# Kernel tuning notes

Hardware: AMD Instinct MI355X
Metric: run time of the kernel (lower is better)

The kernel has to match this reference:

```python
import jax, jax.numpy as jnp
import numpy as np
from jax import lax

K = 8  # number of KNN neighbors (excluding self)


def setup_inputs() -> dict:
    key = jax.random.key(0)
    k1, k2, k3 = jax.random.split(key, 3)
    B, H, W, C = 32, 14, 14, 2048
    OUT = 512
    x = jax.random.normal(k1, (B, H, W, C), dtype=jnp.float32)
    W1 = jax.random.normal(k2, (C, OUT), dtype=jnp.float32) * (1.0 / np.sqrt(C))
    b1 = jnp.zeros((OUT,), dtype=jnp.float32)
    W2 = jax.random.normal(k3, (OUT, OUT), dtype=jnp.float32) * (1.0 / np.sqrt(OUT))
    b2 = jnp.zeros((OUT,), dtype=jnp.float32)
    return {"x": x, "W1": W1, "b1": b1, "W2": W2, "b2": b2}


def _knn_edges(xf, k):
    # full pairwise squared-euclidean distance (monotone in cdist p=2)
    sq = jnp.sum(xf * xf, axis=-1)                      # [N]
    d2 = sq[:, None] + sq[None, :] - 2.0 * (xf @ xf.T)  # [N, N]
    _, idx = lax.top_k(-d2, k + 1)                      # smallest k+1
    knn = idx[:, 1:]                                    # drop self
    N = xf.shape[0]
    src = jnp.repeat(jnp.arange(N), k)
    dst = knn.reshape(-1)
    # GCNConv adds self-loops
    loops = jnp.arange(N)
    src = jnp.concatenate([src, loops])
    dst = jnp.concatenate([dst, loops])
    return src, dst


def _gcn_conv(h, W, b, src, dst, N):
    # PyG GCNConv: sym-normalized aggregation with self-loops
    deg = jax.ops.segment_sum(jnp.ones_like(dst, dtype=h.dtype), dst, num_segments=N)
    dinv = lax.rsqrt(jnp.maximum(deg, 1.0))
    norm = dinv[src] * dinv[dst]                        # [E]
    hw = h @ W                                          # [N, F]
    msg = hw[src] * norm[:, None]                       # gather + scale
    out = jax.ops.segment_sum(msg, dst, num_segments=N) # scatter-add
    return out + b


def reference(x, W1, b1, W2, b2):
    B, H, Wd, C = x.shape
    N = B * H * Wd
    xf = x.reshape(N, C)
    src, dst = _knn_edges(xf, K)
    h = jax.nn.relu(_gcn_conv(xf, W1, b1, src, dst, N))
    # dropout is identity in eval mode
    h = jax.nn.relu(_gcn_conv(h, W2, b2, src, dst, N))
    return h.reshape(B, H, Wd, W2.shape[1])
```

## Files before the change

kernel.cpp:

```cpp
#include <hip/hip_runtime.h>

typedef __attribute__((ext_vector_type(8))) _Float16 half8;
typedef __attribute__((ext_vector_type(4))) _Float16 half4;
typedef __attribute__((ext_vector_type(4))) float f32x4;

#define N_NODES 6272
#define CDIM    2048
#define ODIM    512
#define NPAN    49
#define NSLOT   392
#define GRID_G  1232
#define GATE    0.6f

#define XHI_OFF    0ul
#define CANDV_OFF  25690112ul
#define CANDI_OFF  35524608ul
#define SQ_OFF     40441856ul
#define KNN_OFF    40466944ul
#define DINV_OFF   41520640ul
#define RPTR_OFF   41545728ul
#define COL_OFF    41571072ul
#define W1T_OFF    41796864ul
#define W2T_OFF    43894016ul
#define HW_OFF     CANDV_OFF
#define H1H_OFF    44418304ul

__device__ __forceinline__ void gld_lds16(const void* g, void* l) {
    __builtin_amdgcn_global_load_lds(
        (const __attribute__((address_space(1))) void*)g,
        (__attribute__((address_space(3))) void*)l, 16, 0, 0);
}

__device__ __forceinline__ half8 frag_read(const char* base, int row, int s, int lane) {
    int b = (s * 4 + (lane >> 4)) ^ (row & 7);
    return *(const half8*)(base + row * 128 + b * 16);
}

#define MF(a, b, c) __builtin_amdgcn_mfma_f32_16x16x32_f16(a, b, c, 0, 0, 0)

__global__ __launch_bounds__(256) void prep_kernel(const float* __restrict__ x,
        _Float16* __restrict__ xhi, float* __restrict__ sq,
        const float* __restrict__ W1, _Float16* __restrict__ w1t,
        const float* __restrict__ W2, _Float16* __restrict__ w2t) {
    __shared__ float tile[64][65];
    int bid = blockIdx.x, tid = threadIdx.x;
    if (bid < 1568) {
        int i = bid * 4 + (tid >> 6);
        int t = tid & 63;
        const float* row = x + (size_t)i * CDIM;
        _Float16* hrow = xhi + (size_t)i * CDIM;
        float s = 0.f;
#pragma unroll
        for (int k = 0; k < 8; k++) {
            float4 v = *(const float4*)(row + (k * 64 + t) * 4);
            half4 h;
            h[0] = (_Float16)v.x; h[1] = (_Float16)v.y;
            h[2] = (_Float16)v.z; h[3] = (_Float16)v.w;
            *(half4*)(hrow + (k * 64 + t) * 4) = h;
            s += v.x * v.x + v.y * v.y + v.z * v.z + v.w * v.w;
        }
#pragma unroll
        for (int off = 32; off; off >>= 1) s += __shfl_down(s, off, 64);
        if (t == 0) sq[i] = s;
        return;
    }
    const float* W; _Float16* Wt; int K, N, idx;
    if (bid < 1824) { idx = bid - 1568; W = W1; Wt = w1t; K = CDIM; N = ODIM; }
    else            { idx = bid - 1824; W = W2; Wt = w2t; K = ODIM; N = ODIM; }
    int nkb = K / 64;
    int kb = (idx % nkb) * 64, nb = (idx / nkb) * 64;
    int r = tid >> 2, c0 = (tid & 3) * 16;
#pragma unroll
    for (int u = 0; u < 4; u++) {
        float4 v = *(const float4*)(W + (size_t)(kb + r) * N + nb + c0 + u * 4);
        tile[r][c0 + u * 4 + 0] = v.x; tile[r][c0 + u * 4 + 1] = v.y;
        tile[r][c0 + u * 4 + 2] = v.z; tile[r][c0 + u * 4 + 3] = v.w;
    }
    __syncthreads();
    int rn = tid >> 2, ck0 = (tid & 3) * 16;
#pragma unroll
    for (int u = 0; u < 4; u++) {
        half4 o;
#pragma unroll
        for (int j = 0; j < 4; j++) o[j] = (_Float16)tile[ck0 + u * 4 + j][rn];
        *(half4*)(Wt + (size_t)(nb + rn) * K + kb + ck0 + u * 4) = o;
    }
}

__global__ __launch_bounds__(256, 4) void gram_screen(
        const _Float16* __restrict__ xhi, const float* __restrict__ sq,
        float* __restrict__ candv, unsigned short* __restrict__ candi) {
    __shared__ char lds[32768];
    float* S = (float*)lds;
    float* topv = (float*)(lds + 16896);
    unsigned short* topi = (unsigned short*)(lds + 21504);
#define TOPV(r, k) topv[(r) * 9 + (k)]
#define TOPI(r, k) topi[(r) * 10 + (k)]

    int tid = threadIdx.x, lane = tid & 63, wave = tid >> 6;
    int wr = wave >> 1, wc = wave & 1;
    int l15 = lane & 15, kg = lane >> 4;

    int xcd = blockIdx.x & 7, loc = blockIdx.x >> 3;
    if (xcd != 0 && loc >= 153) return;
    int raster = (xcd == 0) ? loc : (154 + (xcd - 1) * 153 + loc);
    int t = (int)((sqrtf(8.f * (float)raster + 1.f) - 1.f) * 0.5f);
    while ((t + 1) * (t + 2) / 2 <= raster) t++;
    while (t * (t + 1) / 2 > raster) t--;
    int p = raster - t * (t + 1) / 2;
    size_t i0 = (size_t)p * 128, j0 = (size_t)t * 128;

    f32x4 acc[4][4] = {};

    int r_in = lane >> 3;
    int skb = (lane & 7) ^ r_in;

#pragma unroll 1
    for (int c = 0; c < 32; c++) {
        int kk = c * 64;
#pragma unroll
        for (int g = 0; g < 8; g++) {
            int sg = wave * 8 + g;
            int tI = sg >> 4, seg = sg & 15;
            size_t row = (tI ? j0 : i0) + (size_t)(seg * 8 + r_in);
            gld_lds16(xhi + row * CDIM + kk + skb * 8, lds + tI * 16384 + seg * 1024);
        }
        __syncthreads();
#pragma unroll
        for (int s = 0; s < 2; s++) {
            half8 a4[4];
#pragma unroll
            for (int m = 0; m < 4; m++)
                a4[m] = frag_read(lds, wr * 64 + m * 16 + l15, s, lane);
#pragma unroll
            for (int n = 0; n < 4; n++) {
                half8 b = frag_read(lds + 16384, wc * 64 + n * 16 + l15, s, lane);
#pragma unroll
                for (int m = 0; m < 4; m++) acc[m][n] = MF(a4[m], b, acc[m][n]);
            }
        }
        __syncthreads();
    }

    float sqi[4][4];
#pragma unroll
    for (int m = 0; m < 4; m++)
#pragma unroll
        for (int r = 0; r < 4; r++)
            sqi[m][r] = sq[(int)i0 + wr * 64 + m * 16 + kg * 4 + r];
    float sqj[4];
#pragma unroll
    for (int n = 0; n < 4; n++)
        sqj[n] = sq[(int)j0 + wc * 64 + n * 16 + l15];

    if (tid < 128) {
#pragma unroll
        for (int k = 0; k < 8; k++) { TOPV(tid, k) = 3.4e38f; TOPI(tid, k) = 0xFFFF; }
    }

#pragma unroll
    for (int cs = 0; cs < 4; cs++) {
        __syncthreads();
        if (wc == (cs >> 1)) {
            const int n0 = (cs & 1) * 2;
#pragma unroll
            for (int m = 0; m < 4; m++)
#pragma unroll
                for (int nn = 0; nn < 2; nn++)
#pragma unroll
                    for (int r = 0; r < 4; r++) {
                        int row = wr * 64 + m * 16 + kg * 4 + r;
                        float d2 = sqi[m][r] + sqj[n0 + nn] - 2.f * acc[m][n0 + nn][r];
                        S[row * 33 + nn * 16 + l15] = d2;
                    }
        }
        __syncthreads();
        if (tid < 128) {
            int r = tid, gi = (int)i0 + r;
            int cbase = (int)j0 + cs * 32;
#pragma unroll 4
            for (int jj = 0; jj < 32; jj++) {
                int gj = cbase + jj;
                if (gj == gi) continue;
                float v = S[r * 33 + jj];
                float wv = TOPV(r, 7); int wi = TOPI(r, 7);
                if (v < wv || (v == wv && gj < wi)) {
                    int pos = 7;
                    while (pos > 0) {
                        float pv = TOPV(r, pos - 1); int pi = TOPI(r, pos - 1);
                        if (v < pv || (v == pv && gj < pi)) {
                            TOPV(r, pos) = pv; TOPI(r, pos) = (unsigned short)pi; pos--;
                        } else break;
                    }
                    TOPV(r, pos) = v; TOPI(r, pos) = (unsigned short)gj;
                }
            }
        }
    }
    __syncthreads();
    if (tid < 128) {
        int gi = (int)i0 + tid;
#pragma unroll
        for (int k = 0; k < 8; k++) {
            candv[(size_t)gi * NSLOT + t * 8 + k] = TOPV(tid, k);
            candi[(size_t)gi * NSLOT + t * 8 + k] = TOPI(tid, k);
        }
#pragma unroll
        for (int k = 0; k < 8; k++) { TOPV(tid, k) = 3.4e38f; TOPI(tid, k) = 0xFFFF; }
    }

    if (p < t) {
#pragma unroll
        for (int ss = 0; ss < 4; ss++) {
            __syncthreads();
            if (wr == (ss >> 1)) {
                const int mb = (ss & 1) * 2;
#pragma unroll
                for (int mm = 0; mm < 2; mm++)
#pragma unroll
                    for (int n = 0; n < 4; n++)
#pragma unroll
                        for (int r = 0; r < 4; r++) {
                            int rl  = mm * 16 + kg * 4 + r;
                            int col = wc * 64 + n * 16 + l15;
                            float d2 = sqi[mb + mm][r] + sqj[n] - 2.f * acc[mb + mm][n][r];
                            S[col * 33 + rl] = d2;
                        }
            }
            __syncthreads();
            if (tid < 128) {
                int cc = tid;
                int rbase = (int)i0 + ss * 32;
#pragma unroll 4
                for (int jj = 0; jj < 32; jj++) {
                    int gi = rbase + jj;
                    float v = S[cc * 33 + jj];
                    float wv = TOPV(cc, 7); int wi = TOPI(cc, 7);
                    if (v < wv || (v == wv && gi < wi)) {
                        int pos = 7;
                        while (pos > 0) {
                            float pv = TOPV(cc, pos - 1); int pi = TOPI(cc, pos - 1);
                            if (v < pv || (v == pv && gi < pi)) {
                                TOPV(cc, pos) = pv; TOPI(cc, pos) = (unsigned short)pi; pos--;
                            } else break;
                        }
                        TOPV(cc, pos) = v; TOPI(cc, pos) = (unsigned short)gi;
                    }
                }
            }
        }
        __syncthreads();
        if (tid < 128) {
            int gj = (int)j0 + tid;
#pragma unroll
            for (int k = 0; k < 8; k++) {
                candv[(size_t)gj * NSLOT + p * 8 + k] = TOPV(tid, k);
                candi[(size_t)gj * NSLOT + p * 8 + k] = TOPI(tid, k);
            }
        }
    }
#undef TOPV
#undef TOPI
}

__global__ __launch_bounds__(256) void knn_select_kernel(
        const float* __restrict__ candv, const unsigned short* __restrict__ candi,
        const float* __restrict__ x, const float* __restrict__ sq,
        int* __restrict__ knn) {
    int node = blockIdx.x * 4 + (threadIdx.x >> 6);
    int lane = threadIdx.x & 63;
    const float* cv = candv + (size_t)node * NSLOT;
    const unsigned short* ci = candi + (size_t)node * NSLOT;
    float v[7]; int ix[7];
#pragma unroll
    for (int u = 0; u < 7; u++) {
        int s = u * 64 + lane;
        bool ok = (s < NSLOT);
        v[u]  = ok ? cv[s] : 3.4e38f;
        ix[u] = ok ? (int)ci[s] : 0x7fffffff;
    }
    float myv16 = 3.4e38f; int myc = 0x7fffffff;
#pragma unroll 1
    for (int k = 0; k < 16; k++) {
        float bv = v[0]; int bi = ix[0];
#pragma unroll
        for (int u = 1; u < 7; u++)
            if (v[u] < bv || (v[u] == bv && ix[u] < bi)) { bv = v[u]; bi = ix[u]; }
#pragma unroll
        for (int off = 32; off; off >>= 1) {
            float ov = __shfl_xor(bv, off, 64);
            int   oi = __shfl_xor(bi, off, 64);
            if (ov < bv || (ov == bv && oi < bi)) { bv = ov; bi = oi; }
        }
        if (lane == k) { myv16 = bv; myc = bi; }
#pragma unroll
        for (int u = 0; u < 7; u++)
            if (ix[u] == bi) { v[u] = 3.4e38f; ix[u] = 0x7fffffff; }
    }
    float g7 = __shfl(myv16, 7, 64), g8 = __shfl(myv16, 8, 64);
    if (g8 - g7 > GATE) {
        if (lane < 8) knn[(size_t)node * 8 + lane] = myc;
        return;
    }
    const float* xi = x + (size_t)node * CDIM;
    float4 a[8];
#pragma unroll
    for (int g = 0; g < 8; g++) a[g] = *(const float4*)(xi + (g * 64 + lane) * 4);
    float sqi = sq[node];
    float rv = 3.4e38f; int ri = 0x7fffffff;
#pragma unroll 1
    for (int c = 0; c < 16; c++) {
        int j = __shfl(myc, c, 64);
        const float* xj = x + (size_t)j * CDIM;
        float s = 0.f;
#pragma unroll
        for (int g = 0; g < 8; g++) {
            float4 b = *(const float4*)(xj + (g * 64 + lane) * 4);
            s = fmaf(a[g].x, b.x, s); s = fmaf(a[g].y, b.y, s);
            s = fmaf(a[g].z, b.z, s); s = fmaf(a[g].w, b.w, s);
        }
#pragma unroll
        for (int off = 32; off; off >>= 1) s += __shfl_down(s, off, 64);
        float d2 = sqi + sq[j] - 2.f * s;
        d2 = __shfl(d2, 0, 64);
        if (lane == c) { rv = d2; ri = j; }
    }
#pragma unroll 1
    for (int k = 0; k < 8; k++) {
        float bv = rv; int bi = ri;
#pragma unroll
        for (int off = 8; off; off >>= 1) {
            float ov = __shfl_xor(bv, off, 64);
            int   oi = __shfl_xor(bi, off, 64);
            if (ov < bv || (ov == bv && oi < bi)) { bv = ov; bi = oi; }
        }
        bv = __shfl(bv, lane & 15, 64); bi = __shfl(bi, lane & 15, 64);
        if (lane == 0) knn[(size_t)node * 8 + k] = bi;
        if (ri == bi) { rv = 3.4e38f; ri = 0x7fffffff; }
    }
}

__global__ __launch_bounds__(1024) void graph_build_kernel(
        const int* __restrict__ knn, float* __restrict__ dinv,
        int* __restrict__ row_ptr, int* __restrict__ col) {
    __shared__ int deg_l[N_NODES];
    __shared__ int cnt_l[N_NODES];
    __shared__ int rp_l[N_NODES];
    __shared__ int partial[1024];
    int tid = threadIdx.x;
    for (int i = tid; i < N_NODES; i += 1024) { deg_l[i] = 1; cnt_l[i] = 0; }
    __syncthreads();
    for (int e = tid; e < N_NODES * 8; e += 1024) atomicAdd(&deg_l[knn[e]], 1);
    __syncthreads();
    const int CH = 7;
    int start = tid * CH;
    int end = start + CH; if (end > N_NODES) end = N_NODES;
    int s = 0;
    for (int i = start; i < end; i++) s += deg_l[i];
    partial[tid] = s;
    __syncthreads();
    if (tid == 0) {
        int run = 0;
        for (int k = 0; k < 1024; k++) { int vv = partial[k]; partial[k] = run; run += vv; }
        row_ptr[N_NODES] = run;
    }
    __syncthreads();
    int run = partial[tid];
    for (int i = start; i < end; i++) {
        rp_l[i] = run; row_ptr[i] = run;
        dinv[i] = rsqrtf((float)deg_l[i]);
        run += deg_l[i];
    }
    __syncthreads();
    for (int i = tid; i < N_NODES; i += 1024) {
        int p0 = rp_l[i] + atomicAdd(&cnt_l[i], 1);
        col[p0] = i;
#pragma unroll
        for (int j = 0; j < 8; j++) {
            int d = knn[i * 8 + j];
            int q = rp_l[d] + atomicAdd(&cnt_l[d], 1);
            col[q] = i;
        }
    }
}

__global__ __launch_bounds__(256) void hgemm_nt_kernel(
        const _Float16* __restrict__ A, const _Float16* __restrict__ Bt,
        _Float16* __restrict__ C, int M, int N, int K) {
    __shared__ char lds[24576];
    int tid = threadIdx.x, lane = tid & 63, wave = tid >> 6;
    int l15 = lane & 15, kg = lane >> 4;
    int nt = N >> 7;
    int nblk = (M >> 6) * nt;
    int per = nblk >> 3;
    int swz = (blockIdx.x & 7) * per + (blockIdx.x >> 3);
    int i0 = (swz % (M >> 6)) * 64, j0 = (swz / (M >> 6)) * 128;
    f32x4 acc[4][2] = {};

    int r_in = lane >> 3;
    int skb = (lane & 7) ^ r_in;

#pragma unroll 1
    for (int kk = 0; kk < K; kk += 64) {
        __syncthreads();
#pragma unroll
        for (int g = 0; g < 6; g++) {
            int sg = wave * 6 + g;
            if (sg < 8) {
                gld_lds16(A + (size_t)(i0 + sg * 8 + r_in) * K + kk + skb * 8,
                          lds + sg * 1024);
            } else {
                int seg = sg - 8;
                gld_lds16(Bt + (size_t)(j0 + seg * 8 + r_in) * K + kk + skb * 8,
                          lds + 8192 + seg * 1024);
            }
        }
        __syncthreads();
#pragma unroll
        for (int s = 0; s < 2; s++) {
            half8 a[4];
#pragma unroll
            for (int m = 0; m < 4; m++) a[m] = frag_read(lds, m * 16 + l15, s, lane);
#pragma unroll
            for (int n = 0; n < 2; n++) {
                half8 b = frag_read(lds + 8192, wave * 32 + n * 16 + l15, s, lane);
#pragma unroll
                for (int m = 0; m < 4; m++) acc[m][n] = MF(a[m], b, acc[m][n]);
            }
        }
    }
#pragma unroll
    for (int m = 0; m < 4; m++)
#pragma unroll
        for (int n = 0; n < 2; n++)
#pragma unroll
            for (int r = 0; r < 4; r++) {
                int row = i0 + m * 16 + kg * 4 + r;
                int colj = j0 + wave * 32 + n * 16 + l15;
                C[(size_t)row * N + colj] = (_Float16)acc[m][n][r];
            }
}

template <bool HALF_OUT>
__global__ __launch_bounds__(256) void aggregate_kernel(
        const _Float16* __restrict__ hw, const int* __restrict__ row_ptr,
        const int* __restrict__ col, const float* __restrict__ dinv,
        const float* __restrict__ bias, void* __restrict__ outp) {
    int node = blockIdx.x * 4 + (threadIdx.x >> 6);
    int lane = threadIdx.x & 63;
    int e0 = row_ptr[node], e1 = row_ptr[node + 1];
    float acc[8] = {};
    for (int e = e0; e < e1; e++) {
        int s = col[e];
        float w = dinv[s];
        half8 v = *(const half8*)(hw + (size_t)s * ODIM + lane * 8);
#pragma unroll
        for (int j = 0; j < 8; j++) acc[j] = fmaf(w, (float)v[j], acc[j]);
    }
    float wd = dinv[node];
    float4 b0 = *(const float4*)(bias + lane * 8);
    float4 b1 = *(const float4*)(bias + lane * 8 + 4);
    float o[8];
    o[0] = fmaxf(fmaf(acc[0], wd, b0.x), 0.f);
    o[1] = fmaxf(fmaf(acc[1], wd, b0.y), 0.f);
    o[2] = fmaxf(fmaf(acc[2], wd, b0.z), 0.f);
    o[3] = fmaxf(fmaf(acc[3], wd, b0.w), 0.f);
    o[4] = fmaxf(fmaf(acc[4], wd, b1.x), 0.f);
    o[5] = fmaxf(fmaf(acc[5], wd, b1.y), 0.f);
    o[6] = fmaxf(fmaf(acc[6], wd, b1.z), 0.f);
    o[7] = fmaxf(fmaf(acc[7], wd, b1.w), 0.f);
    if (HALF_OUT) {
        half8 h;
#pragma unroll
        for (int j = 0; j < 8; j++) h[j] = (_Float16)o[j];
        *(half8*)((_Float16*)outp + (size_t)node * ODIM + lane * 8) = h;
    } else {
        float* out = (float*)outp;
        float4 f0 = {o[0], o[1], o[2], o[3]}, f1 = {o[4], o[5], o[6], o[7]};
        *(float4*)(out + (size_t)node * ODIM + lane * 8)     = f0;
        *(float4*)(out + (size_t)node * ODIM + lane * 8 + 4) = f1;
    }
}

extern "C" void kernel_launch(void* const* d_in, const int* in_sizes, int n_in,
                              void* d_out, int out_size, void* d_ws, size_t ws_size,
                              hipStream_t stream) {
    const float* x  = (const float*)d_in[0];
    const float* W1 = (const float*)d_in[1];
    const float* b1 = (const float*)d_in[2];
    const float* W2 = (const float*)d_in[3];
    const float* b2 = (const float*)d_in[4];
    float* out = (float*)d_out;
    char* ws = (char*)d_ws;

    _Float16* xhi  = (_Float16*)(ws + XHI_OFF);
    float* candv   = (float*)(ws + CANDV_OFF);
    unsigned short* candi = (unsigned short*)(ws + CANDI_OFF);
    float* sq      = (float*)(ws + SQ_OFF);
    int*   knn     = (int*)  (ws + KNN_OFF);
    float* dinv    = (float*)(ws + DINV_OFF);
    int*   row_ptr = (int*)  (ws + RPTR_OFF);
    int*   col     = (int*)  (ws + COL_OFF);
    _Float16* w1t  = (_Float16*)(ws + W1T_OFF);
    _Float16* w2t  = (_Float16*)(ws + W2T_OFF);
    _Float16* hw   = (_Float16*)(ws + HW_OFF);
    _Float16* h1h  = (_Float16*)(ws + H1H_OFF);

    prep_kernel<<<1888, 256, 0, stream>>>(x, xhi, sq, W1, w1t, W2, w2t);
    gram_screen<<<GRID_G, 256, 0, stream>>>(xhi, sq, candv, candi);
    knn_select_kernel<<<N_NODES / 4, 256, 0, stream>>>(candv, candi, x, sq, knn);
    graph_build_kernel<<<1, 1024, 0, stream>>>(knn, dinv, row_ptr, col);

    hgemm_nt_kernel<<<(N_NODES / 64) * (ODIM / 128), 256, 0, stream>>>(xhi, w1t, hw, N_NODES, ODIM, CDIM);
    aggregate_kernel<true><<<N_NODES / 4, 256, 0, stream>>>(hw, row_ptr, col, dinv, b1, (void*)h1h);
    hgemm_nt_kernel<<<(N_NODES / 64) * (ODIM / 128), 256, 0, stream>>>(h1h, w2t, hw, N_NODES, ODIM, ODIM);
    aggregate_kernel<false><<<N_NODES / 4, 256, 0, stream>>>(hw, row_ptr, col, dinv, b2, (void*)out);
}
```

Before: 1.131 ms.

## Fuse layer-1 feature GEMM into the Gram screening launch as extra blocks

The X·W1 half-precision GEMM no longer runs as its own launch after graph building. Its tiles are appended as extra blocks to the Gram/KNN screening kernel, so both independent GEMMs share one launch and can fill the GPU together. The hw buffer moves to its own workspace region because it no longer aliases the candidate buffers that the screening blocks are still writing. The cost is a larger combined grid that may compete for CUs and cache, and the tail of the screening work could be lengthened.

```diff
diff --git a/kernel.cpp b/kernel.cpp
--- a/kernel.cpp
+++ b/kernel.cpp
@@ -10,6 +10,7 @@
 #define NPAN    49
 #define NSLOT   392
 #define GRID_G  1232
+#define GRID_H1 392
 #define GATE    0.6f
 
 #define XHI_OFF    0ul
@@ -22,8 +23,8 @@
 #define COL_OFF    41571072ul
 #define W1T_OFF    41796864ul
 #define W2T_OFF    43894016ul
-#define HW_OFF     CANDV_OFF
 #define H1H_OFF    44418304ul
+#define HW_OFF     50843648ul
 
 __device__ __forceinline__ void gld_lds16(const void* g, void* l) {
     __builtin_amdgcn_global_load_lds(
@@ -87,19 +88,71 @@
     }
 }
 
-__global__ __launch_bounds__(256, 4) void gram_screen(
+__global__ __launch_bounds__(256, 4) void gram_hgemm_kernel(
         const _Float16* __restrict__ xhi, const float* __restrict__ sq,
-        float* __restrict__ candv, unsigned short* __restrict__ candi) {
+        float* __restrict__ candv, unsigned short* __restrict__ candi,
+        const _Float16* __restrict__ w1t, _Float16* __restrict__ hw) {
     __shared__ char lds[32768];
+    int tid = threadIdx.x, lane = tid & 63, wave = tid >> 6;
+    int l15 = lane & 15, kg = lane >> 4;
+    int r_in = lane >> 3;
+    int skb = (lane & 7) ^ r_in;
+
+    if (blockIdx.x >= GRID_G) {
+        int hb = blockIdx.x - GRID_G;
+        const int nit = N_NODES / 64;
+        int per = GRID_H1 >> 3;
+        int swz = (hb & 7) * per + (hb >> 3);
+        int i0 = (swz % nit) * 64, j0 = (swz / nit) * 128;
+        f32x4 acc[4][2] = {};
+#pragma unroll 1
+        for (int kk = 0; kk < CDIM; kk += 64) {
+            __syncthreads();
+#pragma unroll
+            for (int g = 0; g < 6; g++) {
+                int sg = wave * 6 + g;
+                if (sg < 8) {
+                    gld_lds16(xhi + (size_t)(i0 + sg * 8 + r_in) * CDIM + kk + skb * 8,
+                              lds + sg * 1024);
+                } else {
+                    int seg = sg - 8;
+                    gld_lds16(w1t + (size_t)(j0 + seg * 8 + r_in) * CDIM + kk + skb * 8,
+                              lds + 8192 + seg * 1024);
+                }
+            }
+            __syncthreads();
+#pragma unroll
+            for (int s = 0; s < 2; s++) {
+                half8 a[4];
+#pragma unroll
+                for (int m = 0; m < 4; m++) a[m] = frag_read(lds, m * 16 + l15, s, lane);
+#pragma unroll
+                for (int n = 0; n < 2; n++) {
+                    half8 b = frag_read(lds + 8192, wave * 32 + n * 16 + l15, s, lane);
+#pragma unroll
+                    for (int m = 0; m < 4; m++) acc[m][n] = MF(a[m], b, acc[m][n]);
+                }
+            }
+        }
+#pragma unroll
+        for (int m = 0; m < 4; m++)
+#pragma unroll
+            for (int n = 0; n < 2; n++)
+#pragma unroll
+                for (int r = 0; r < 4; r++) {
+                    int row = i0 + m * 16 + kg * 4 + r;
+                    int colj = j0 + wave * 32 + n * 16 + l15;
+                    hw[(size_t)row * ODIM + colj] = (_Float16)acc[m][n][r];
+                }
+        return;
+    }
+
     float* S = (float*)lds;
     float* topv = (float*)(lds + 16896);
     unsigned short* topi = (unsigned short*)(lds + 21504);
 #define TOPV(r, k) topv[(r) * 9 + (k)]
 #define TOPI(r, k) topi[(r) * 10 + (k)]
-
-    int tid = threadIdx.x, lane = tid & 63, wave = tid >> 6;
     int wr = wave >> 1, wc = wave & 1;
-    int l15 = lane & 15, kg = lane >> 4;
 
     int xcd = blockIdx.x & 7, loc = blockIdx.x >> 3;
     if (xcd != 0 && loc >= 153) return;
@@ -111,9 +164,6 @@
     size_t i0 = (size_t)p * 128, j0 = (size_t)t * 128;
 
     f32x4 acc[4][4] = {};
-
-    int r_in = lane >> 3;
-    int skb = (lane & 7) ^ r_in;
 
 #pragma unroll 1
     for (int c = 0; c < 32; c++) {
@@ -507,11 +557,10 @@
     _Float16* h1h  = (_Float16*)(ws + H1H_OFF);
 
     prep_kernel<<<1888, 256, 0, stream>>>(x, xhi, sq, W1, w1t, W2, w2t);
-    gram_screen<<<GRID_G, 256, 0, stream>>>(xhi, sq, candv, candi);
+    gram_hgemm_kernel<<<GRID_G + GRID_H1, 256, 0, stream>>>(xhi, sq, candv, candi, w1t, hw);
     knn_select_kernel<<<N_NODES / 4, 256, 0, stream>>>(candv, candi, x, sq, knn);
     graph_build_kernel<<<1, 1024, 0, stream>>>(knn, dinv, row_ptr, col);
 
-    hgemm_nt_kernel<<<(N_NODES / 64) * (ODIM / 128), 256, 0, stream>>>(xhi, w1t, hw, N_NODES, ODIM, CDIM);
     aggregate_kernel<true><<<N_NODES / 4, 256, 0, stream>>>(hw, row_ptr, col, dinv, b1, (void*)h1h);
     hgemm_nt_kernel<<<(N_NODES / 64) * (ODIM / 128), 256, 0, stream>>>(h1h, w2t, hw, N_NODES, ODIM, ODIM);
     aggregate_kernel<false><<<N_NODES / 4, 256, 0, stream>>>(hw, row_ptr, col, dinv, b2, (void*)out);
```

Measured after the change: 1.100 ms. 2.8% less time.
